# Kernel optimization log

Hardware: AMD Instinct MI355X
Metric: run time of the kernel (lower is better)

The kernel has to match this reference:

```python
import jax, jax.numpy as jnp
import numpy as np

N = 100_000   # nodes
E = 6_400_000  # edges (avg degree 64)
K = 3          # TAGConv hops -> K+1 linear terms per layer


def setup_inputs() -> dict:
    key = jax.random.key(0)
    ks = jax.random.split(key, 9)
    return {
        "x": jax.random.normal(ks[0], (N,), jnp.float32),
        "edge_index": jax.random.randint(ks[1], (2, E), 0, N, jnp.int32),
        "edge_attr": jax.random.normal(ks[2], (E,), jnp.float32),
        "k": 5000,
        "W1": jax.random.normal(ks[3], (K + 1, 1, 8), jnp.float32) * 0.5,
        "b1": jax.random.normal(ks[4], (8,), jnp.float32) * 0.1,
        "W2": jax.random.normal(ks[5], (K + 1, 8, 8), jnp.float32) * 0.2,
        "b2": jax.random.normal(ks[6], (8,), jnp.float32) * 0.1,
        "W3": jax.random.normal(ks[7], (K + 1, 8, 1), jnp.float32) * 0.2,
        "b3": jax.random.normal(ks[8], (1,), jnp.float32) * 0.1,
    }


def _gcn_norm(src, dst, edge_weight, num_nodes):
    # PyG gcn_norm with add_self_loops=False: deg over target index,
    # norm_e = d^{-1/2}[src] * w_e * d^{-1/2}[dst]
    deg = jax.ops.segment_sum(edge_weight, dst, num_segments=num_nodes)
    dis = jnp.where(deg > 0, jax.lax.rsqrt(jnp.where(deg > 0, deg, 1.0)), 0.0)
    return dis[src] * edge_weight * dis[dst]


def _tagconv(x, W, b, src, dst, norm, num_nodes):
    # out = sum_{h=0..K} (A_norm^h x) @ W[h] + b
    out = x @ W[0]
    h = x
    for i in range(1, W.shape[0]):
        h = jax.ops.segment_sum(norm[:, None] * h[src], dst, num_segments=num_nodes)
        out = out + h @ W[i]
    return out + b


def reference(x, edge_index, edge_attr, k, W1, b1, W2, b2, W3, b3):
    num_nodes = x.shape[0]
    x = x[:, None]  # [N, 1]
    src, dst = edge_index[0], edge_index[1]
    norm = _gcn_norm(src, dst, jnp.abs(edge_attr), num_nodes)

    x = jax.nn.relu(_tagconv(x, W1, b1, src, dst, norm, num_nodes))
    x = jax.nn.relu(_tagconv(x, W2, b2, src, dst, norm, num_nodes))
    x = jax.nn.relu(_tagconv(x, W3, b3, src, dst, norm, num_nodes))

    # tg.nn.InstanceNorm(1), batch=None, affine=False: normalize over all nodes
    mean = jnp.mean(x)
    var = jnp.mean((x - mean) ** 2)
    x = ((x - mean) * jax.lax.rsqrt(var + 1e-5)).squeeze(-1)  # [N]

    # top-k one-hot mask (argsort descending -> first k indices)
    _, top_idx = jax.lax.top_k(x, k)
    top_vec = jnp.zeros_like(x).at[top_idx].set(1.0)
    return jnp.column_stack((x, top_vec))  # [N, 2]
```

## Files before the change

kernel.cpp:

```cpp
#include <hip/hip_runtime.h>

#define BS 256
#define BSB 512
#define BSF 1024
#define GPN 16
#define NBLKB 1024
#define BSH 8
#define SMAX 400

static __device__ __forceinline__ float relu_(float v) { return fmaxf(v, 0.0f); }


__global__ void k_binhist(const int* __restrict__ dst, int* __restrict__ bcnt,
                          int E, int chunk, int nbuck) {
  __shared__ int h[1024];
  int b = blockIdx.x, t = threadIdx.x;
  for (int i = t; i < nbuck; i += BSB) h[i] = 0;
  __syncthreads();
  int beg = b * chunk, end = min(E, beg + chunk);
  for (int e = beg + t; e < end; e += BSB) atomicAdd(&h[dst[e] >> BSH], 1);
  __syncthreads();
  for (int i = t; i < nbuck; i += BSB) bcnt[(size_t)i * NBLKB + b] = h[i];
}

__global__ void k_bucketscan(int* __restrict__ bcnt, int* __restrict__ btot) {
  __shared__ int sh[BS];
  int bkt = blockIdx.x, t = threadIdx.x;
  size_t base = (size_t)bkt * NBLKB;
  int c[4], s = 0;
#pragma unroll
  for (int j = 0; j < 4; ++j) { c[j] = bcnt[base + t * 4 + j]; s += c[j]; }
  sh[t] = s; __syncthreads();
  for (int off = 1; off < BS; off <<= 1) {
    int add = (t >= off) ? sh[t - off] : 0; __syncthreads();
    sh[t] += add; __syncthreads();
  }
  int run = sh[t] - s;
#pragma unroll
  for (int j = 0; j < 4; ++j) { bcnt[base + t * 4 + j] = run; run += c[j]; }
  if (t == BS - 1) btot[bkt] = run;
}

__global__ void k_basescan(const int* __restrict__ btot, int* __restrict__ bbase, int nbuck) {
  __shared__ int sh[BS];
  int t = threadIdx.x;
  int run = 0;
  for (int c = 0; c < nbuck; c += BS) {
    int i = c + t;
    int v = (i < nbuck) ? btot[i] : 0;
    sh[t] = v; __syncthreads();
    for (int off = 1; off < BS; off <<= 1) {
      int add = (t >= off) ? sh[t - off] : 0; __syncthreads();
      sh[t] += add; __syncthreads();
    }
    if (i < nbuck) bbase[i] = run + sh[t] - v;
    run += sh[BS - 1];
    __syncthreads();
  }
}

__global__ void k_bin(const int* __restrict__ src, const int* __restrict__ dst,
                      const float* __restrict__ attr, const int* __restrict__ bcnt,
                      const int* __restrict__ bbase, int2* __restrict__ bed,
                      int E, int chunk, int nbuck) {
  __shared__ int2 stage[SMAX][8];
  __shared__ int  fc[SMAX];
  __shared__ int  cur[SMAX];
  int b = blockIdx.x, t = threadIdx.x;
  for (int i = t; i < nbuck; i += BSB) {
    cur[i] = bbase[i] + bcnt[(size_t)i * NBLKB + b];
    fc[i] = 0;
  }
  __syncthreads();
  int beg = b * chunk, end = min(E, beg + chunk);
  for (int base = beg; base < end; base += BSB) {
    int e = base + t;
    if (e < end) {
      int d = dst[e];
      int bkt = d >> BSH;
      int2 rec = make_int2((int)(((unsigned)(d & ((1 << BSH) - 1)) << 17) | (unsigned)src[e]),
                           __float_as_int(fabsf(attr[e])));
      int slot = atomicAdd(&fc[bkt], 1);
      if (slot < 8) stage[bkt][slot] = rec;
      else { int gp = atomicAdd(&cur[bkt], 1); bed[gp] = rec; }
    }
    __syncthreads();
    for (int i = t; i < nbuck; i += BSB) {
      int c = fc[i]; if (c > 8) c = 8;
      if (c == 8) {
        int gp = cur[i]; cur[i] = gp + 8;
#pragma unroll
        for (int j = 0; j < 8; ++j) bed[gp + j] = stage[i][j];
        fc[i] = 0;
      }
    }
    __syncthreads();
  }
  for (int i = t; i < nbuck; i += BSB) {
    int c = fc[i]; if (c > 8) c = 8;
    if (c) {
      int gp = cur[i];
      for (int j = 0; j < c; ++j) bed[gp + j] = stage[i][j];
    }
  }
}

__global__ void k_cntfill(const int2* __restrict__ bed, const int* __restrict__ bbase,
                          const int* __restrict__ btot, const float* __restrict__ x,
                          float* __restrict__ dis, float* __restrict__ xhat,
                          int* __restrict__ rowptr, int2* __restrict__ adj, int N, int E) {
  __shared__ int2  stage[1 << BSH][16];
  __shared__ int   lc[1 << BSH];
  __shared__ float ld[1 << BSH];
  __shared__ int   sc[1 << BSH];
  __shared__ int   fc[1 << BSH];
  __shared__ int   rcur[1 << BSH];
  int bkt = blockIdx.x, t = threadIdx.x;
  if (t < (1 << BSH)) { lc[t] = 0; ld[t] = 0.f; }
  __syncthreads();
  int beg = bbase[bkt], tot = btot[bkt];
  for (int i = t; i < tot; i += BSF) {
    int2 rec = bed[beg + i];
    int dl = (int)((unsigned)rec.x >> 17);
    atomicAdd(&lc[dl], 1);
    atomicAdd(&ld[dl], __int_as_float(rec.y));
  }
  __syncthreads();
  if (t < (1 << BSH)) sc[t] = lc[t];
  __syncthreads();
  for (int off = 1; off < (1 << BSH); off <<= 1) {
    int add = 0;
    if (t < (1 << BSH) && t >= off) add = sc[t - off];
    __syncthreads();
    if (t < (1 << BSH)) sc[t] += add;
    __syncthreads();
  }
  if (t < (1 << BSH)) {
    int myrow = beg + sc[t] - lc[t];
    rcur[t] = myrow;
    fc[t] = 0;
    int n = (bkt << BSH) + t;
    if (n < N) {
      rowptr[n] = myrow;
      float dg = ld[t];
      float d = (dg > 0.f) ? (1.0f / sqrtf(dg)) : 0.f;
      dis[n] = d;
      xhat[n] = d * x[n];
    }
  }
  if (bkt == (int)gridDim.x - 1 && t == 0) rowptr[N] = E;
  __syncthreads();
  for (int base = 0; base < tot; base += BSF) {
    int i = base + t;
    if (i < tot) {
      int2 rec = bed[beg + i];
      unsigned u = (unsigned)rec.x;
      int dl = (int)(u >> 17);
      int2 orec = make_int2((int)(u & 0x1FFFFu), rec.y);
      int slot = atomicAdd(&fc[dl], 1);
      if (slot < 16) stage[dl][slot] = orec;
      else { int gp = atomicAdd(&rcur[dl], 1); adj[gp] = orec; }
    }
    __syncthreads();
    if (t < (1 << BSH)) {
      int c = fc[t]; if (c > 16) c = 16;
      if (c == 16) {
        int gp = rcur[t]; rcur[t] = gp + 16;
#pragma unroll
        for (int j = 0; j < 16; ++j) adj[gp + j] = stage[t][j];
        fc[t] = 0;
      }
    }
    __syncthreads();
  }
  if (t < (1 << BSH)) {
    int c = fc[t]; if (c > 16) c = 16;
    if (c) {
      int gp = rcur[t];
      for (int j = 0; j < c; ++j) adj[gp + j] = stage[t][j];
    }
  }
}


__global__ void k_scanA(const int* __restrict__ cnt, int* __restrict__ bsum, int N) {
  __shared__ int sh[BS];
  int t = threadIdx.x;
  int base = blockIdx.x * 1024;
  int s = 0;
#pragma unroll
  for (int j = 0; j < 4; ++j) { int i = base + t * 4 + j; s += (i < N) ? cnt[i] : 0; }
  sh[t] = s; __syncthreads();
  for (int off = 128; off; off >>= 1) { if (t < off) sh[t] += sh[t + off]; __syncthreads(); }
  if (t == 0) bsum[blockIdx.x] = sh[0];
}

__global__ void k_scanB(int* __restrict__ bsum, int NB2) {
  __shared__ int sh[BS];
  int t = threadIdx.x;
  int v = (t < NB2) ? bsum[t] : 0;
  sh[t] = v; __syncthreads();
  for (int off = 1; off < BS; off <<= 1) {
    int add = (t >= off) ? sh[t - off] : 0; __syncthreads();
    sh[t] += add; __syncthreads();
  }
  if (t < NB2) bsum[t] = sh[t] - v;
}

__global__ void k_scanC(const int* __restrict__ cnt, const int* __restrict__ bsum,
                        int* __restrict__ rowptr, int* __restrict__ cursor, int N, int E) {
  __shared__ int sh[BS];
  int b = blockIdx.x, t = threadIdx.x;
  int base = b * 1024;
  int c[4]; int s = 0;
#pragma unroll
  for (int j = 0; j < 4; ++j) { int i = base + t * 4 + j; c[j] = (i < N) ? cnt[i] : 0; s += c[j]; }
  sh[t] = s; __syncthreads();
  for (int off = 1; off < BS; off <<= 1) {
    int add = (t >= off) ? sh[t - off] : 0; __syncthreads();
    sh[t] += add; __syncthreads();
  }
  int run = sh[t] - s + bsum[b];
#pragma unroll
  for (int j = 0; j < 4; ++j) {
    int i = base + t * 4 + j;
    if (i < N) { rowptr[i] = run; if (cursor) cursor[i] = run; run += c[j]; }
  }
  if (b == 0 && t == 0) rowptr[N] = E;
}

__global__ void k_count(const int* __restrict__ dst, int* __restrict__ cnt, int E) {
  int e = blockIdx.x * blockDim.x + threadIdx.x;
  if (e < E) atomicAdd(&cnt[dst[e]], 1);
}

__global__ void k_place(const int* __restrict__ src, const int* __restrict__ dst,
                        const float* __restrict__ attr, int* __restrict__ cursor,
                        int2* __restrict__ adj, int E) {
  int e = blockIdx.x * blockDim.x + threadIdx.x;
  if (e >= E) return;
  int d = dst[e];
  int pos = atomicAdd(&cursor[d], 1);
  adj[pos] = make_int2(src[e], __float_as_int(fabsf(attr[e])));
}

__global__ void k_degdis(const int* __restrict__ rowptr, const int2* __restrict__ adj,
                         const float* __restrict__ x, float* __restrict__ dis,
                         float* __restrict__ xhat, int N) {
  int g = (blockIdx.x * blockDim.x + threadIdx.x) / GPN;
  int l = threadIdx.x & (GPN - 1);
  if (g >= N) return;
  int beg = rowptr[g], end = rowptr[g + 1];
  float s = 0.0f;
  for (int e = beg + l; e < end; e += GPN) s += __int_as_float(adj[e].y);
#pragma unroll
  for (int off = 8; off; off >>= 1) s += __shfl_xor(s, off, GPN);
  if (l == 0) {
    float d = (s > 0.0f) ? (1.0f / sqrtf(s)) : 0.0f;
    dis[g] = d;
    xhat[g] = d * x[g];
  }
}


static __device__ __forceinline__ float edge_sum1(const int2* __restrict__ adj,
                                                  const float* __restrict__ uin,
                                                  int beg, int end, int l) {
  float acc0 = 0.0f, acc1 = 0.0f;
  int e = beg + l;
  int last = end - GPN;
  for (; e < last; e += 2 * GPN) {
    int2 s0 = adj[e], s1 = adj[e + GPN];
    acc0 += __int_as_float(s0.y) * uin[s0.x];
    acc1 += __int_as_float(s1.y) * uin[s1.x];
  }
  if (e < end) { int2 s0 = adj[e]; acc0 += __int_as_float(s0.y) * uin[s0.x]; }
  float acc = acc0 + acc1;
#pragma unroll
  for (int off = 8; off; off >>= 1) acc += __shfl_xor(acc, off, GPN);
  return acc;
}

__global__ void k_gp1_uh(const int* __restrict__ rowptr, const int2* __restrict__ adj,
                         const float* __restrict__ uin, const float* __restrict__ dis,
                         float* __restrict__ hout, float* __restrict__ uout, int N) {
  int g = (blockIdx.x * blockDim.x + threadIdx.x) / GPN;
  int l = threadIdx.x & (GPN - 1);
  if (g >= N) return;
  float acc = edge_sum1(adj, uin, rowptr[g], rowptr[g + 1], l);
  if (l == 0) {
    float d = dis[g];
    float h = d * acc;
    hout[g] = h;
    uout[g] = d * h;
  }
}

__global__ void k_gp1_y(const int* __restrict__ rowptr, const int2* __restrict__ adj,
                        const float* __restrict__ u2, const float* __restrict__ x,
                        const float* __restrict__ h1, const float* __restrict__ h2,
                        const float* __restrict__ dis, const float* __restrict__ W1,
                        const float* __restrict__ b1, const float* __restrict__ W23,
                        float* __restrict__ y, float* __restrict__ Phat, int N) {
  int g = (blockIdx.x * blockDim.x + threadIdx.x) / GPN;
  int l = threadIdx.x & (GPN - 1);
  if (g >= N) return;
  float acc = edge_sum1(adj, u2, rowptr[g], rowptr[g + 1], l);
  if (l == 0) {
    float d = dis[g];
    float xv = x[g], a = h1[g], b = h2[g], c = d * acc;
    float o[8];
#pragma unroll
    for (int j = 0; j < 8; ++j)
      o[j] = relu_(xv * W1[j] + a * W1[8 + j] + b * W1[16 + j] + c * W1[24 + j] + b1[j]);
    float4* op = (float4*)(y + (size_t)g * 8);
    op[0] = make_float4(o[0], o[1], o[2], o[3]);
    op[1] = make_float4(o[4], o[5], o[6], o[7]);
    float p[8];
#pragma unroll
    for (int j = 0; j < 8; ++j) {
      float s = 0.0f;
#pragma unroll
      for (int i = 0; i < 8; ++i) s += o[i] * W23[i * 8 + j];
      p[j] = d * s;
    }
    float4* pp = (float4*)(Phat + (size_t)g * 8);
    pp[0] = make_float4(p[0], p[1], p[2], p[3]);
    pp[1] = make_float4(p[4], p[5], p[6], p[7]);
  }
}

#define EDGE_SUM8(ADJ, UIN, BEG, END, L)                                        \
  float a0=0,a1=0,a2=0,a3=0,a4=0,a5=0,a6=0,a7=0;                                \
  {                                                                             \
    int e = (BEG) + (L);                                                        \
    int last = (END) - GPN;                                                     \
    for (; e < last; e += 2 * GPN) {                                            \
      int2 s0 = (ADJ)[e], s1 = (ADJ)[e + GPN];                                  \
      float w0 = __int_as_float(s0.y), w1 = __int_as_float(s1.y);               \
      const float4* p0 = (const float4*)((UIN) + (size_t)s0.x * 8);             \
      const float4* p1 = (const float4*)((UIN) + (size_t)s1.x * 8);             \
      float4 u0 = p0[0], v0 = p0[1], u1 = p1[0], v1 = p1[1];                    \
      a0 += w0*u0.x; a1 += w0*u0.y; a2 += w0*u0.z; a3 += w0*u0.w;               \
      a4 += w0*v0.x; a5 += w0*v0.y; a6 += w0*v0.z; a7 += w0*v0.w;               \
      a0 += w1*u1.x; a1 += w1*u1.y; a2 += w1*u1.z; a3 += w1*u1.w;               \
      a4 += w1*v1.x; a5 += w1*v1.y; a6 += w1*v1.z; a7 += w1*v1.w;               \
    }                                                                           \
    if (e < (END)) {                                                            \
      int2 s0 = (ADJ)[e];                                                       \
      float w0 = __int_as_float(s0.y);                                          \
      const float4* p0 = (const float4*)((UIN) + (size_t)s0.x * 8);             \
      float4 u0 = p0[0], v0 = p0[1];                                            \
      a0 += w0*u0.x; a1 += w0*u0.y; a2 += w0*u0.z; a3 += w0*u0.w;               \
      a4 += w0*v0.x; a5 += w0*v0.y; a6 += w0*v0.z; a7 += w0*v0.w;               \
    }                                                                           \
  }                                                                             \
  _Pragma("unroll")                                                             \
  for (int off = 8; off; off >>= 1) {                                           \
    a0 += __shfl_xor(a0, off, GPN); a1 += __shfl_xor(a1, off, GPN);             \
    a2 += __shfl_xor(a2, off, GPN); a3 += __shfl_xor(a3, off, GPN);             \
    a4 += __shfl_xor(a4, off, GPN); a5 += __shfl_xor(a5, off, GPN);             \
    a6 += __shfl_xor(a6, off, GPN); a7 += __shfl_xor(a7, off, GPN);             \
  }

__global__ void k_gp8_u(const int* __restrict__ rowptr, const int2* __restrict__ adj,
                        const float* __restrict__ uin, const float* __restrict__ y,
                        const float* __restrict__ W, const float* __restrict__ dis,
                        float* __restrict__ uout, int N) {
  int g = (blockIdx.x * blockDim.x + threadIdx.x) / GPN;
  int l = threadIdx.x & (GPN - 1);
  if (g >= N) return;
  int beg = rowptr[g], end = rowptr[g + 1];
  EDGE_SUM8(adj, uin, beg, end, l)
  if (l == 0) {
    float d = dis[g];
    const float4* yp = (const float4*)(y + (size_t)g * 8);
    float4 u = yp[0], v = yp[1];
    float yi[8] = {u.x, u.y, u.z, u.w, v.x, v.y, v.z, v.w};
    float acc[8] = {a0, a1, a2, a3, a4, a5, a6, a7};
    float o[8];
#pragma unroll
    for (int j = 0; j < 8; ++j) {
      float s = 0.0f;
#pragma unroll
      for (int i = 0; i < 8; ++i) s += yi[i] * W[i * 8 + j];
      o[j] = d * (s + d * acc[j]);
    }
    float4* op = (float4*)(uout + (size_t)g * 8);
    op[0] = make_float4(o[0], o[1], o[2], o[3]);
    op[1] = make_float4(o[4], o[5], o[6], o[7]);
  }
}

__global__ void k_gp8_fin(const int* __restrict__ rowptr, const int2* __restrict__ adj,
                          const float* __restrict__ uin, const float* __restrict__ y,
                          const float* __restrict__ W0, const float* __restrict__ b2,
                          const float* __restrict__ W3, const float* __restrict__ dis,
                          float* __restrict__ S3hat, float* __restrict__ B2,
                          float* __restrict__ B1, float* __restrict__ B0, int N) {
  int g = (blockIdx.x * blockDim.x + threadIdx.x) / GPN;
  int l = threadIdx.x & (GPN - 1);
  if (g >= N) return;
  int beg = rowptr[g], end = rowptr[g + 1];
  EDGE_SUM8(adj, uin, beg, end, l)
  if (l == 0) {
    float d = dis[g];
    const float4* yp = (const float4*)(y + (size_t)g * 8);
    float4 u = yp[0], v = yp[1];
    float yi[8] = {u.x, u.y, u.z, u.w, v.x, v.y, v.z, v.w};
    float acc[8] = {a0, a1, a2, a3, a4, a5, a6, a7};
    float z[8];
#pragma unroll
    for (int j = 0; j < 8; ++j) {
      float s = 0.0f;
#pragma unroll
      for (int i = 0; i < 8; ++i) s += yi[i] * W0[i * 8 + j];
      z[j] = relu_(s + d * acc[j] + b2[j]);
    }
    float tt[4];
#pragma unroll
    for (int i = 0; i < 4; ++i) {
      float s = 0.0f;
#pragma unroll
      for (int j = 0; j < 8; ++j) s += z[j] * W3[i * 8 + j];
      tt[i] = s;
    }
    B0[g] = tt[0]; B1[g] = tt[1]; B2[g] = tt[2];
    S3hat[g] = d * tt[3];
  }
}

__global__ void k_gp1_bu(const int* __restrict__ rowptr, const int2* __restrict__ adj,
                         const float* __restrict__ uin, const float* __restrict__ B,
                         const float* __restrict__ dis, float* __restrict__ uout, int N) {
  int g = (blockIdx.x * blockDim.x + threadIdx.x) / GPN;
  int l = threadIdx.x & (GPN - 1);
  if (g >= N) return;
  float acc = edge_sum1(adj, uin, rowptr[g], rowptr[g + 1], l);
  if (l == 0) {
    float d = dis[g];
    uout[g] = d * (B[g] + d * acc);
  }
}

__global__ void k_gp1_last(const int* __restrict__ rowptr, const int2* __restrict__ adj,
                           const float* __restrict__ uin, const float* __restrict__ B0,
                           const float* __restrict__ b3, const float* __restrict__ dis,
                           float* __restrict__ r, unsigned* __restrict__ keys,
                           double* __restrict__ partials, int N) {
  __shared__ double s1[BS];
  __shared__ double s2[BS];
  int tid = blockIdx.x * blockDim.x + threadIdx.x;
  int g = tid / GPN, l = tid & (GPN - 1);
  float rv = 0.0f;
  bool writer = false;
  if (g < N) {
    float acc = edge_sum1(adj, uin, rowptr[g], rowptr[g + 1], l);
    if (l == 0) {
      float gg = B0[g] + dis[g] * acc;
      rv = relu_(gg + b3[0]);
      r[g] = rv;
      keys[g] = __float_as_uint(rv) | 0x80000000u;
      writer = true;
    }
  }
  double v = writer ? (double)rv : 0.0;
  s1[threadIdx.x] = v;
  s2[threadIdx.x] = v * v;
  __syncthreads();
  for (int off = 128; off; off >>= 1) {
    if (threadIdx.x < off) {
      s1[threadIdx.x] += s1[threadIdx.x + off];
      s2[threadIdx.x] += s2[threadIdx.x + off];
    }
    __syncthreads();
  }
  if (threadIdx.x == 0) {
    partials[2 * (size_t)blockIdx.x]     = s1[0];
    partials[2 * (size_t)blockIdx.x + 1] = s2[0];
  }
}

__global__ void k_stats(const double* __restrict__ partials, int nparts,
                        float* __restrict__ stats, int N) {
  __shared__ double s1[BS];
  __shared__ double s2[BS];
  int t = threadIdx.x;
  double a = 0.0, b = 0.0;
  for (int i = t; i < nparts; i += BS) { a += partials[2 * (size_t)i]; b += partials[2 * (size_t)i + 1]; }
  s1[t] = a; s2[t] = b;
  __syncthreads();
  for (int off = 128; off; off >>= 1) {
    if (t < off) { s1[t] += s1[t + off]; s2[t] += s2[t + off]; }
    __syncthreads();
  }
  if (t == 0) {
    double mean = s1[0] / (double)N;
    double var  = s2[0] / (double)N - mean * mean;
    stats[0] = (float)mean;
    stats[1] = (float)(1.0 / sqrt(var + 1e-5));
  }
}


__global__ void k_stateinit(unsigned* __restrict__ state, const int* __restrict__ kp) {
  state[0] = 0u;
  state[1] = (unsigned)kp[0];
}

__global__ void k_hist(const unsigned* __restrict__ keys, int N,
                       const unsigned* __restrict__ state, unsigned* __restrict__ hist,
                       int shift) {
  __shared__ unsigned sh[256];
  sh[threadIdx.x] = 0;
  __syncthreads();
  unsigned prefix = state[0];
  unsigned hmask = (shift >= 24) ? 0u : (0xFFFFFFFFu << (shift + 8));
  int stride = gridDim.x * blockDim.x;
  for (int n = blockIdx.x * blockDim.x + threadIdx.x; n < N; n += stride) {
    unsigned kk = keys[n];
    if ((kk & hmask) == (prefix & hmask)) atomicAdd(&sh[(kk >> shift) & 255u], 1u);
  }
  __syncthreads();
  atomicAdd(&hist[threadIdx.x], sh[threadIdx.x]);
}

__global__ void k_select(unsigned* __restrict__ state, unsigned* __restrict__ hist, int shift) {
  __shared__ unsigned sh[BS];
  int t = threadIdx.x;
  unsigned c = hist[t];
  sh[t] = c;
  __syncthreads();
  for (int off = 1; off < BS; off <<= 1) {
    unsigned add = (t + off < BS) ? sh[t + off] : 0u; __syncthreads();
    sh[t] += add; __syncthreads();
  }
  unsigned rem = state[1];
  unsigned S = sh[t];
  if (S >= rem && (S - c) < rem) {
    state[0] |= ((unsigned)t) << shift;
    state[1] = rem - (S - c);
  }
  hist[t] = 0;
}

__global__ void k_mark(const unsigned* __restrict__ keys, const float* __restrict__ r,
                       const float* __restrict__ stats, int N,
                       const unsigned* __restrict__ state, float* __restrict__ out,
                       unsigned* __restrict__ blkcnt) {
  unsigned T = state[0];
  float mean = stats[0], istd = stats[1];
  int n = blockIdx.x * 256 + threadIdx.x;
  int eq = 0;
  __shared__ int sh;
  if (threadIdx.x == 0) sh = 0;
  __syncthreads();
  if (n < N) {
    out[2 * (size_t)n] = (r[n] - mean) * istd;
    unsigned kk = keys[n];
    out[2 * (size_t)n + 1] = (kk > T) ? 1.0f : 0.0f;
    eq = (kk == T);
  }
  if (eq) atomicAdd(&sh, 1);
  __syncthreads();
  if (threadIdx.x == 0) blkcnt[blockIdx.x] = (unsigned)sh;
}

__global__ void k_scanP(const unsigned* __restrict__ blkcnt, unsigned* __restrict__ scanbuf, int NB) {
  __shared__ unsigned sh[BS];
  int t = threadIdx.x;
  unsigned c0 = (2 * t < NB) ? blkcnt[2 * t] : 0u;
  unsigned c1 = (2 * t + 1 < NB) ? blkcnt[2 * t + 1] : 0u;
  unsigned s = c0 + c1;
  sh[t] = s; __syncthreads();
  for (int off = 1; off < BS; off <<= 1) {
    unsigned add = (t >= off) ? sh[t - off] : 0u; __syncthreads();
    sh[t] += add; __syncthreads();
  }
  unsigned ex = sh[t] - s;
  if (2 * t < NB) scanbuf[2 * t] = ex;
  if (2 * t + 1 < NB) scanbuf[2 * t + 1] = ex + c0;
}

__global__ void k_resolve(const unsigned* __restrict__ keys, int N,
                          const unsigned* __restrict__ state,
                          const unsigned* __restrict__ scanbuf, float* __restrict__ out) {
  unsigned T = state[0];
  unsigned m = state[1];
  int n = blockIdx.x * 256 + threadIdx.x;
  if (n >= N) return;
  if (keys[n] != T) return;
  unsigned rank = scanbuf[blockIdx.x];
  int base = blockIdx.x * 256;
  for (int j = base; j < n; ++j) rank += (keys[j] == T);
  out[2 * (size_t)n + 1] = (rank < m) ? 1.0f : 0.0f;
}


extern "C" void kernel_launch(void* const* d_in, const int* in_sizes, int n_in,
                              void* d_out, int out_size, void* d_ws, size_t ws_size,
                              hipStream_t stream) {
  const float* x    = (const float*)d_in[0];
  const int*   ei   = (const int*)d_in[1];
  const float* attr = (const float*)d_in[2];
  const int*   kp   = (const int*)d_in[3];
  const float* W1   = (const float*)d_in[4];
  const float* b1   = (const float*)d_in[5];
  const float* W2   = (const float*)d_in[6];
  const float* b2   = (const float*)d_in[7];
  const float* W3   = (const float*)d_in[8];
  const float* b3   = (const float*)d_in[9];
  const int N = in_sizes[0];
  const int E = in_sizes[2];
  const int* src = ei;
  const int* dst = ei + E;
  float* out = (float*)d_out;
  const int NB    = (N + 255) / 256;
  const int NB2   = (N + 1023) / 1024;
  const int NBUCK = (N + (1 << BSH) - 1) >> BSH;
  const int chunk = (E + NBLKB - 1) / NBLKB;
  const int GGB   = (int)(((size_t)N * GPN + BS - 1) / BS);

  char* p = (char*)d_ws;
  auto alloc = [&](size_t bytes) -> char* {
    char* r = p; p += (bytes + 255) & ~(size_t)255; return r;
  };
  float*    dis    = (float*)alloc((size_t)N * 4);
  float*    xhat   = (float*)alloc((size_t)N * 4);
  float*    h1     = (float*)alloc((size_t)N * 4);
  float*    h2     = (float*)alloc((size_t)N * 4);
  float*    u1     = (float*)alloc((size_t)N * 4);
  float*    u2     = (float*)alloc((size_t)N * 4);
  float*    y      = (float*)alloc((size_t)N * 32);
  float*    Phat   = (float*)alloc((size_t)N * 32);
  float*    Qhat   = (float*)alloc((size_t)N * 32);
  float*    S3hat  = (float*)alloc((size_t)N * 4);
  float*    B2     = (float*)alloc((size_t)N * 4);
  float*    B1     = (float*)alloc((size_t)N * 4);
  float*    B0     = (float*)alloc((size_t)N * 4);
  float*    g2hat  = (float*)alloc((size_t)N * 4);
  float*    g1hat  = (float*)alloc((size_t)N * 4);
  float*    r      = (float*)alloc((size_t)N * 4);
  unsigned* keys   = (unsigned*)alloc((size_t)N * 4);
  double*   parts  = (double*)alloc((size_t)GGB * 16);
  float*    stats  = (float*)alloc(8);
  unsigned* state  = (unsigned*)alloc(8);
  unsigned* hist   = (unsigned*)alloc(1024);
  unsigned* blkcnt = (unsigned*)alloc((size_t)NB * 4);
  unsigned* scanbf = (unsigned*)alloc((size_t)NB * 4);
  int*      rowptr = (int*)alloc((size_t)(N + 1) * 4);
  int*      cursor = (int*)alloc((size_t)N * 4);
  int*      cnt    = (int*)alloc((size_t)N * 4);
  int*      bsum   = (int*)alloc(2048);
  int2*     adj    = (int2*)alloc((size_t)E * 8);
  int2*     bed    = (int2*)alloc((size_t)E * 8);
  int*      bcnt   = (int*)alloc((size_t)NBUCK * NBLKB * 4);
  int*      btot   = (int*)alloc((size_t)NBUCK * 4 + 256);
  int*      bbase  = (int*)alloc((size_t)NBUCK * 4 + 256);
  size_t need_new = (size_t)(p - (char*)d_ws);

  dim3 B(BS);
  int genb = (E + BS - 1) / BS;
  dim3 GE(genb), GG(GGB), GN(NB), GB(NBUCK);

  bool use_new = (need_new <= ws_size) && (N <= 102400) && (NBUCK <= SMAX);

  hipMemsetAsync(hist, 0, 1024, stream);

  if (use_new) {
    k_binhist<<<dim3(NBLKB), dim3(BSB), 0, stream>>>(dst, bcnt, E, chunk, NBUCK);
    k_bucketscan<<<GB, B, 0, stream>>>(bcnt, btot);
    k_basescan<<<dim3(1), B, 0, stream>>>(btot, bbase, NBUCK);
    k_bin<<<dim3(NBLKB), dim3(BSB), 0, stream>>>(src, dst, attr, bcnt, bbase, bed, E, chunk, NBUCK);
    k_cntfill<<<GB, dim3(BSF), 0, stream>>>(bed, bbase, btot, x, dis, xhat, rowptr, adj, N, E);
  } else {
    hipMemsetAsync(cnt, 0, (size_t)N * 4, stream);
    k_count<<<GE, B, 0, stream>>>(dst, cnt, E);
    k_scanA<<<dim3(NB2), B, 0, stream>>>(cnt, bsum, N);
    k_scanB<<<dim3(1), B, 0, stream>>>(bsum, NB2);
    k_scanC<<<dim3(NB2), B, 0, stream>>>(cnt, bsum, rowptr, cursor, N, E);
    k_place<<<GE, B, 0, stream>>>(src, dst, attr, cursor, adj, E);
    k_degdis<<<GG, B, 0, stream>>>(rowptr, adj, x, dis, xhat, N);
  }

  k_gp1_uh<<<GG, B, 0, stream>>>(rowptr, adj, xhat, dis, h1, u1, N);
  k_gp1_uh<<<GG, B, 0, stream>>>(rowptr, adj, u1, dis, h2, u2, N);
  k_gp1_y<<<GG, B, 0, stream>>>(rowptr, adj, u2, x, h1, h2, dis, W1, b1, W2 + 3 * 64, y, Phat, N);

  k_gp8_u<<<GG, B, 0, stream>>>(rowptr, adj, Phat, y, W2 + 2 * 64, dis, Qhat, N);
  k_gp8_u<<<GG, B, 0, stream>>>(rowptr, adj, Qhat, y, W2 + 1 * 64, dis, Phat, N);
  k_gp8_fin<<<GG, B, 0, stream>>>(rowptr, adj, Phat, y, W2, b2, W3, dis, S3hat, B2, B1, B0, N);

  k_gp1_bu<<<GG, B, 0, stream>>>(rowptr, adj, S3hat, B2, dis, g2hat, N);
  k_gp1_bu<<<GG, B, 0, stream>>>(rowptr, adj, g2hat, B1, dis, g1hat, N);
  k_gp1_last<<<GG, B, 0, stream>>>(rowptr, adj, g1hat, B0, b3, dis, r, keys, parts, N);

  k_stats<<<dim3(1), B, 0, stream>>>(parts, GGB, stats, N);

  k_stateinit<<<dim3(1), dim3(1), 0, stream>>>(state, kp);
  for (int shift = 24; shift >= 0; shift -= 8) {
    k_hist<<<GN, B, 0, stream>>>(keys, N, state, hist, shift);
    k_select<<<dim3(1), B, 0, stream>>>(state, hist, shift);
  }
  k_mark<<<GN, B, 0, stream>>>(keys, r, stats, N, state, out, blkcnt);
  k_scanP<<<dim3(1), B, 0, stream>>>(blkcnt, scanbf, NB);
  k_resolve<<<GN, B, 0, stream>>>(keys, N, state, scanbf, out);
}
```

Before: 533.0 us.

## Simplify CSR fill scatter, unroll edge gather by four, fold state init

The per-bucket CSR fill kernel drops its shared-memory staging of 16-record batches and instead scatters each edge directly to adj through a shared-memory atomic cursor. The single-channel edge gather loop goes from 2 to 4 independent accumulators to expose more memory-level parallelism. The selection state init is folded into k_stats, removing one kernel launch. The bin kernel's staging array is padded to 9 columns to reduce LDS bank conflicts. Direct scatter gives less coalesced writes to adj but fewer barriers and less LDS use.

```diff
diff --git a/kernel.cpp b/kernel.cpp
--- a/kernel.cpp
+++ b/kernel.cpp
@@ -63,7 +63,7 @@
                       const float* __restrict__ attr, const int* __restrict__ bcnt,
                       const int* __restrict__ bbase, int2* __restrict__ bed,
                       int E, int chunk, int nbuck) {
-  __shared__ int2 stage[SMAX][8];
+  __shared__ int2 stage[SMAX][9];
   __shared__ int  fc[SMAX];
   __shared__ int  cur[SMAX];
   int b = blockIdx.x, t = threadIdx.x;
@@ -109,11 +109,9 @@
                           const int* __restrict__ btot, const float* __restrict__ x,
                           float* __restrict__ dis, float* __restrict__ xhat,
                           int* __restrict__ rowptr, int2* __restrict__ adj, int N, int E) {
-  __shared__ int2  stage[1 << BSH][16];
   __shared__ int   lc[1 << BSH];
   __shared__ float ld[1 << BSH];
   __shared__ int   sc[1 << BSH];
-  __shared__ int   fc[1 << BSH];
   __shared__ int   rcur[1 << BSH];
   int bkt = blockIdx.x, t = threadIdx.x;
   if (t < (1 << BSH)) { lc[t] = 0; ld[t] = 0.f; }
@@ -138,7 +136,6 @@
   if (t < (1 << BSH)) {
     int myrow = beg + sc[t] - lc[t];
     rcur[t] = myrow;
-    fc[t] = 0;
     int n = (bkt << BSH) + t;
     if (n < N) {
       rowptr[n] = myrow;
@@ -150,35 +147,12 @@
   }
   if (bkt == (int)gridDim.x - 1 && t == 0) rowptr[N] = E;
   __syncthreads();
-  for (int base = 0; base < tot; base += BSF) {
-    int i = base + t;
-    if (i < tot) {
-      int2 rec = bed[beg + i];
-      unsigned u = (unsigned)rec.x;
-      int dl = (int)(u >> 17);
-      int2 orec = make_int2((int)(u & 0x1FFFFu), rec.y);
-      int slot = atomicAdd(&fc[dl], 1);
-      if (slot < 16) stage[dl][slot] = orec;
-      else { int gp = atomicAdd(&rcur[dl], 1); adj[gp] = orec; }
-    }
-    __syncthreads();
-    if (t < (1 << BSH)) {
-      int c = fc[t]; if (c > 16) c = 16;
-      if (c == 16) {
-        int gp = rcur[t]; rcur[t] = gp + 16;
-#pragma unroll
-        for (int j = 0; j < 16; ++j) adj[gp + j] = stage[t][j];
-        fc[t] = 0;
-      }
-    }
-    __syncthreads();
-  }
-  if (t < (1 << BSH)) {
-    int c = fc[t]; if (c > 16) c = 16;
-    if (c) {
-      int gp = rcur[t];
-      for (int j = 0; j < c; ++j) adj[gp + j] = stage[t][j];
-    }
+  for (int i = t; i < tot; i += BSF) {
+    int2 rec = bed[beg + i];
+    unsigned u = (unsigned)rec.x;
+    int dl = (int)(u >> 17);
+    int pos = atomicAdd(&rcur[dl], 1);
+    adj[pos] = make_int2((int)(u & 0x1FFFFu), rec.y);
   }
 }
 
@@ -266,16 +240,17 @@
 static __device__ __forceinline__ float edge_sum1(const int2* __restrict__ adj,
                                                   const float* __restrict__ uin,
                                                   int beg, int end, int l) {
-  float acc0 = 0.0f, acc1 = 0.0f;
+  float a0 = 0.f, a1 = 0.f, a2 = 0.f, a3 = 0.f;
   int e = beg + l;
-  int last = end - GPN;
-  for (; e < last; e += 2 * GPN) {
-    int2 s0 = adj[e], s1 = adj[e + GPN];
-    acc0 += __int_as_float(s0.y) * uin[s0.x];
-    acc1 += __int_as_float(s1.y) * uin[s1.x];
-  }
-  if (e < end) { int2 s0 = adj[e]; acc0 += __int_as_float(s0.y) * uin[s0.x]; }
-  float acc = acc0 + acc1;
+  for (; e + 3 * GPN < end; e += 4 * GPN) {
+    int2 s0 = adj[e], s1 = adj[e + GPN], s2 = adj[e + 2 * GPN], s3 = adj[e + 3 * GPN];
+    a0 += __int_as_float(s0.y) * uin[s0.x];
+    a1 += __int_as_float(s1.y) * uin[s1.x];
+    a2 += __int_as_float(s2.y) * uin[s2.x];
+    a3 += __int_as_float(s3.y) * uin[s3.x];
+  }
+  for (; e < end; e += GPN) { int2 s0 = adj[e]; a0 += __int_as_float(s0.y) * uin[s0.x]; }
+  float acc = (a0 + a1) + (a2 + a3);
 #pragma unroll
   for (int off = 8; off; off >>= 1) acc += __shfl_xor(acc, off, GPN);
   return acc;
@@ -482,7 +457,8 @@
 }
 
 __global__ void k_stats(const double* __restrict__ partials, int nparts,
-                        float* __restrict__ stats, int N) {
+                        float* __restrict__ stats, unsigned* __restrict__ state,
+                        const int* __restrict__ kp, int N) {
   __shared__ double s1[BS];
   __shared__ double s2[BS];
   int t = threadIdx.x;
@@ -499,14 +475,11 @@
     double var  = s2[0] / (double)N - mean * mean;
     stats[0] = (float)mean;
     stats[1] = (float)(1.0 / sqrt(var + 1e-5));
-  }
-}
-
-
-__global__ void k_stateinit(unsigned* __restrict__ state, const int* __restrict__ kp) {
-  state[0] = 0u;
-  state[1] = (unsigned)kp[0];
-}
+    state[0] = 0u;
+    state[1] = (unsigned)kp[0];
+  }
+}
+
 
 __global__ void k_hist(const unsigned* __restrict__ keys, int N,
                        const unsigned* __restrict__ state, unsigned* __restrict__ hist,
@@ -695,9 +668,8 @@
   k_gp1_bu<<<GG, B, 0, stream>>>(rowptr, adj, g2hat, B1, dis, g1hat, N);
   k_gp1_last<<<GG, B, 0, stream>>>(rowptr, adj, g1hat, B0, b3, dis, r, keys, parts, N);
 
-  k_stats<<<dim3(1), B, 0, stream>>>(parts, GGB, stats, N);
-
-  k_stateinit<<<dim3(1), dim3(1), 0, stream>>>(state, kp);
+  k_stats<<<dim3(1), B, 0, stream>>>(parts, GGB, stats, state, kp, N);
+
   for (int shift = 24; shift >= 0; shift -= 8) {
     k_hist<<<GN, B, 0, stream>>>(keys, N, state, hist, shift);
     k_select<<<dim3(1), B, 0, stream>>>(state, hist, shift);
```

Result: no change. 539.7 us (median of 2 runs) (+1.2%).
